# Performance work log

Hardware: AMD Instinct MI355X
Metric: run time of the kernel (lower is better)

Reference implementation:

```python
import jax, jax.numpy as jnp
import numpy as np

B, P, M = 16, 16384, 2048
D_Z, D_PHI, D_R = 512, 256, 64
H1, H2 = 96, 96
IN_DIM = D_Z + 3 * D_PHI + D_R  # 1344


def setup_inputs() -> dict:
    key = jax.random.key(0)
    ks = jax.random.split(key, 8)
    g_q = jax.random.normal(ks[0], (B, D_Z), dtype=jnp.float32)
    Phi = jax.random.normal(ks[1], (M, D_PHI), dtype=jnp.float32)
    # pair indices with i < j (sort each row)
    pi = jax.random.randint(ks[2], (P, 2), 0, M, dtype=jnp.int64)
    pair_index = jnp.sort(pi, axis=-1)
    relation_features = jax.random.normal(ks[3], (P, D_R), dtype=jnp.float32)
    # learned MLP params (Linear weights stored [in, out])
    W1 = jax.random.normal(ks[4], (IN_DIM, H1), dtype=jnp.float32) / np.sqrt(IN_DIM)
    b1 = jnp.zeros((H1,), dtype=jnp.float32)
    W2 = jax.random.normal(ks[5], (H1, H2), dtype=jnp.float32) / np.sqrt(H1)
    b2 = jnp.zeros((H2,), dtype=jnp.float32)
    W3 = jax.random.normal(ks[6], (H2, 1), dtype=jnp.float32) / np.sqrt(H2)
    b3 = jnp.zeros((1,), dtype=jnp.float32)
    return {"g_q": g_q, "Phi": Phi, "pair_index": pair_index,
            "relation_features": relation_features,
            "W1": W1, "b1": b1, "W2": W2, "b2": b2, "W3": W3, "b3": b3}


def reference(g_q, Phi, pair_index, relation_features, W1, b1, W2, b2, W3, b3):
    # gather pair embeddings: [P, d_phi]
    phi_i = Phi[pair_index[:, 0]]
    phi_j = Phi[pair_index[:, 1]]
    # symmetric combine -> [P, 3*d_phi + d_r]
    pair_feats = jnp.concatenate(
        [phi_i + phi_j, jnp.abs(phi_i - phi_j), phi_i * phi_j, relation_features],
        axis=-1)
    b, p = g_q.shape[0], pair_feats.shape[0]
    # broadcast-concat -> x: [B, P, in_dim]
    x = jnp.concatenate(
        [jnp.broadcast_to(g_q[:, None, :], (b, p, g_q.shape[-1])),
         jnp.broadcast_to(pair_feats[None, :, :], (b, p, pair_feats.shape[-1]))],
        axis=-1)
    # small MLP: Linear -> GELU (erf, dropout is identity at eval) x2, then Linear(->1)
    h = jax.nn.gelu(x @ W1 + b1, approximate=False)
    h = jax.nn.gelu(h @ W2 + b2, approximate=False)
    out = h @ W3 + b3  # [B, P, 1]
    return out[..., 0]  # [B, P]
```

## Files before the change

### kernel.cpp

```cpp
#include <hip/hip_runtime.h>
#include <hip/hip_bf16.h>
#include <stdint.h>

static constexpr int P_N   = 16384;
static constexpr int D_Z   = 512;
static constexpr int D_PHI = 256;
static constexpr int D_R   = 64;
static constexpr int H     = 96;
static constexpr int KP    = 832;

using f32x4 = __attribute__((ext_vector_type(4))) float;
using s16x8 = __attribute__((ext_vector_type(8))) short;

__device__ __forceinline__ unsigned short f2bf(float f) {
    union { float f; uint32_t u; } v; v.f = f;
    return (unsigned short)((v.u + 0x7FFFu + ((v.u >> 16) & 1u)) >> 16);
}

__device__ __forceinline__ uint32_t pkbf2(float lo, float hi) {
    union { __hip_bfloat162 h; uint32_t u; } c;
    c.h = __float22bfloat162_rn(make_float2(lo, hi));
    return c.u;
}

__device__ __forceinline__ float gelu_f(float x) {
    float x2 = x * x;
    float u  = __builtin_fmaf(-0.1029444f, x2, -2.3022126f);
    float e  = __builtin_amdgcn_exp2f(x * u);
    return x * __builtin_amdgcn_rcpf(1.0f + e);
}

__global__ __launch_bounds__(256) void prep_kernel(
    const float* __restrict__ g_q, const float* __restrict__ W1,
    const float* __restrict__ b1, const float* __restrict__ W2,
    float* __restrict__ gqfrag, unsigned short* __restrict__ W1frag,
    unsigned short* __restrict__ W2frag)
{
    __shared__ float gql[D_Z];
    __shared__ float red[192];
    const int blk = blockIdx.x;
    const int t = threadIdx.x;
    if (blk < 16) {
        const int b = blk;
        for (int i = t; i < D_Z; i += 256) gql[i] = g_q[b * D_Z + i];
        __syncthreads();
        float acc = 0.f;
        if (t < 192) {
            const int n = t % 96, s = t / 96;
            const int k0 = s * 256;
            #pragma unroll 8
            for (int k = 0; k < 256; ++k)
                acc += gql[k0 + k] * W1[(k0 + k) * H + n];
            red[t] = acc;
        }
        __syncthreads();
        if (t < 96) {
            const float v = red[t] + red[t + 96] + b1[t];
            const int dst = ((t >> 5) * 64 + ((t >> 3) & 3) * 16 + b) * 8 + (t & 7);
            gqfrag[dst] = v;
        }
    } else if (blk < 328) {
        const int e = (blk - 16) * 256 + t;
        const int n = e / KP, k = e % KP;
        const int nf = n >> 4, lr = n & 15;
        const int kc = k >> 5, l4 = (k >> 3) & 3, ke = k & 7;
        W1frag[((nf * 26 + kc) * 64 + l4 * 16 + lr) * 8 + ke] =
            f2bf(W1[(D_Z + k) * H + n]);
    } else {
        const int e = (blk - 328) * 256 + t;
        const int n = e / H, k = e % H;
        const int nf = n >> 4, lr = n & 15;
        const int ks = k >> 5, l4 = (k >> 3) & 3, ke = k & 7;
        W2frag[((nf * 3 + ks) * 64 + l4 * 16 + lr) * 8 + ke] =
            f2bf(W2[k * H + n]);
    }
}

__global__ __launch_bounds__(256, 4) void fused5_kernel(
    const float* __restrict__ Phi, const int* __restrict__ pidx,
    const float* __restrict__ rel, const unsigned short* __restrict__ W1frag,
    const float* __restrict__ gqfrag, const unsigned short* __restrict__ W2frag,
    const float* __restrict__ b2, const float* __restrict__ W3,
    const float* __restrict__ b3, float* __restrict__ out)
{
    constexpr int FS = 840;
    __shared__ __align__(16) unsigned short feats[8 * FS];
    __shared__ __align__(16) float y1part[2][8][96];
    const int t = threadIdx.x;
    const int p0 = blockIdx.x * 8;

    for (int task = t; task < 832; task += 256) {
        const int pair = task / 104;
        const int k = (task - pair * 104) * 8;
        float f[8];
        if (k < 768) {
            const int2 ij = *(const int2*)(pidx + 2 * (p0 + pair));
            const int kb = k & 255;
            const float* PI = Phi + ij.x * D_PHI + kb;
            const float* PJ = Phi + ij.y * D_PHI + kb;
            float4 a0 = *(const float4*)PI, a1 = *(const float4*)(PI + 4);
            float4 c0 = *(const float4*)PJ, c1 = *(const float4*)(PJ + 4);
            if (k < 256) {
                f[0]=a0.x+c0.x; f[1]=a0.y+c0.y; f[2]=a0.z+c0.z; f[3]=a0.w+c0.w;
                f[4]=a1.x+c1.x; f[5]=a1.y+c1.y; f[6]=a1.z+c1.z; f[7]=a1.w+c1.w;
            } else if (k < 512) {
                f[0]=fabsf(a0.x-c0.x); f[1]=fabsf(a0.y-c0.y); f[2]=fabsf(a0.z-c0.z); f[3]=fabsf(a0.w-c0.w);
                f[4]=fabsf(a1.x-c1.x); f[5]=fabsf(a1.y-c1.y); f[6]=fabsf(a1.z-c1.z); f[7]=fabsf(a1.w-c1.w);
            } else {
                f[0]=a0.x*c0.x; f[1]=a0.y*c0.y; f[2]=a0.z*c0.z; f[3]=a0.w*c0.w;
                f[4]=a1.x*c1.x; f[5]=a1.y*c1.y; f[6]=a1.z*c1.z; f[7]=a1.w*c1.w;
            }
        } else {
            const float* R = rel + (p0 + pair) * D_R + (k - 768);
            float4 a0 = *(const float4*)R, a1 = *(const float4*)(R + 4);
            f[0]=a0.x; f[1]=a0.y; f[2]=a0.z; f[3]=a0.w;
            f[4]=a1.x; f[5]=a1.y; f[6]=a1.z; f[7]=a1.w;
        }
        uint4 pk;
        pk.x = pkbf2(f[0], f[1]);
        pk.y = pkbf2(f[2], f[3]);
        pk.z = pkbf2(f[4], f[5]);
        pk.w = pkbf2(f[6], f[7]);
        *(uint4*)&feats[pair * FS + k] = pk;
    }
    __syncthreads();

    const int w  = t >> 6;
    const int l  = t & 63;
    const int lr = l & 15, l4 = l >> 4;

    {
        const int kh = w & 1, ng = w >> 1;
        f32x4 acc[3];
        acc[0] = (f32x4){0.f,0.f,0.f,0.f};
        acc[1] = (f32x4){0.f,0.f,0.f,0.f};
        acc[2] = (f32x4){0.f,0.f,0.f,0.f};
        const unsigned short* Arow = &feats[(lr & 7) * FS + l4 * 8];
        const int kc0 = kh * 13;
        for (int i = 0; i < 13; ++i) {
            const int kc = kc0 + i;
            const s16x8 a = *(const s16x8*)(Arow + kc * 32);
            #pragma unroll
            for (int j = 0; j < 3; ++j) {
                const s16x8 bb = *(const s16x8*)(W1frag +
                    (((ng * 3 + j) * 26 + kc) * 64 + l) * 8);
                acc[j] = __builtin_amdgcn_mfma_f32_16x16x32_bf16(a, bb, acc[j], 0, 0, 0);
            }
        }
        if (l4 < 2) {
            #pragma unroll
            for (int j = 0; j < 3; ++j)
                #pragma unroll
                for (int r = 0; r < 4; ++r)
                    y1part[kh][l4 * 4 + r][ng * 48 + j * 16 + lr] = acc[j][r];
        }
    }
    __syncthreads();

    s16x8 afr[2][3];
    #pragma unroll
    for (int ks = 0; ks < 3; ++ks) {
        const int c = ks * 32 + l4 * 8;
        const float* gp = gqfrag + (ks * 64 + l) * 8;
        float4 g0 = *(const float4*)gp, g1 = *(const float4*)(gp + 4);
        #pragma unroll
        for (int mf = 0; mf < 2; ++mf) {
            const int pl = 2 * w + mf;
            const float* ya = &y1part[0][pl][c];
            const float* yb = &y1part[1][pl][c];
            float4 u0 = *(const float4*)ya, u1 = *(const float4*)(ya + 4);
            float4 v0 = *(const float4*)yb, v1 = *(const float4*)(yb + 4);
            union { s16x8 v; uint32_t u[4]; } pk;
            pk.u[0] = pkbf2(gelu_f(g0.x + u0.x + v0.x), gelu_f(g0.y + u0.y + v0.y));
            pk.u[1] = pkbf2(gelu_f(g0.z + u0.z + v0.z), gelu_f(g0.w + u0.w + v0.w));
            pk.u[2] = pkbf2(gelu_f(g1.x + u1.x + v1.x), gelu_f(g1.y + u1.y + v1.y));
            pk.u[3] = pkbf2(gelu_f(g1.z + u1.z + v1.z), gelu_f(g1.w + u1.w + v1.w));
            afr[mf][ks] = pk.v;
        }
    }

    f32x4 acc2[2][6];
    #pragma unroll
    for (int nf = 0; nf < 6; ++nf) {
        const float bv = b2[nf * 16 + lr];
        acc2[0][nf] = (f32x4){bv, bv, bv, bv};
        acc2[1][nf] = (f32x4){bv, bv, bv, bv};
    }
    #pragma unroll
    for (int ks = 0; ks < 3; ++ks) {
        #pragma unroll
        for (int nf = 0; nf < 6; ++nf) {
            const s16x8 bb = *(const s16x8*)(W2frag + ((nf * 3 + ks) * 64 + l) * 8);
            acc2[0][nf] = __builtin_amdgcn_mfma_f32_16x16x32_bf16(afr[0][ks], bb, acc2[0][nf], 0, 0, 0);
            acc2[1][nf] = __builtin_amdgcn_mfma_f32_16x16x32_bf16(afr[1][ks], bb, acc2[1][nf], 0, 0, 0);
        }
    }

    float part[2][4] = {{0.f,0.f,0.f,0.f},{0.f,0.f,0.f,0.f}};
    #pragma unroll
    for (int nf = 0; nf < 6; ++nf) {
        const float wv = W3[nf * 16 + lr];
        #pragma unroll
        for (int mf = 0; mf < 2; ++mf)
            #pragma unroll
            for (int r4 = 0; r4 < 4; ++r4)
                part[mf][r4] = __builtin_fmaf(gelu_f(acc2[mf][nf][r4]), wv, part[mf][r4]);
    }
    #pragma unroll
    for (int mask = 1; mask <= 8; mask <<= 1)
        #pragma unroll
        for (int mf = 0; mf < 2; ++mf)
            #pragma unroll
            for (int r4 = 0; r4 < 4; ++r4)
                part[mf][r4] += __shfl_xor(part[mf][r4], mask, 64);
    if (lr == 0) {
        const float b3v = b3[0];
        #pragma unroll
        for (int mf = 0; mf < 2; ++mf)
            #pragma unroll
            for (int r4 = 0; r4 < 4; ++r4)
                out[(l4 * 4 + r4) * P_N + p0 + 2 * w + mf] = part[mf][r4] + b3v;
    }
}

extern "C" void kernel_launch(void* const* d_in, const int* in_sizes, int n_in,
                              void* d_out, int out_size, void* d_ws, size_t ws_size,
                              hipStream_t stream)
{
    const float* g_q  = (const float*)d_in[0];
    const float* Phi  = (const float*)d_in[1];
    const int*   pidx = (const int*)d_in[2];
    const float* rel  = (const float*)d_in[3];
    const float* W1   = (const float*)d_in[4];
    const float* b1   = (const float*)d_in[5];
    const float* W2   = (const float*)d_in[6];
    const float* b2   = (const float*)d_in[7];
    const float* W3   = (const float*)d_in[8];
    const float* b3   = (const float*)d_in[9];
    float* out = (float*)d_out;

    char* ws = (char*)d_ws;
    float*          gqfrag = (float*)(ws + 0);
    unsigned short* W1frag = (unsigned short*)(ws + 8192);
    unsigned short* W2frag = (unsigned short*)(ws + 167936);

    hipLaunchKernelGGL(prep_kernel, dim3(364), dim3(256), 0, stream,
                       g_q, W1, b1, W2, gqfrag, W1frag, W2frag);
    hipLaunchKernelGGL(fused5_kernel, dim3(P_N / 8), dim3(256), 0, stream,
                       Phi, pidx, rel, W1frag, gqfrag, W2frag, b2, W3, b3, out);
}
```

Before: 46.68 us.

## Split fused kernel into pair-side layer-1 GEMM and separate MLP kernel

Splits the fused kernel in two. The first kernel gathers features for 16 pairs per block, so all 16 rows of each MFMA tile are used (previously only 8). Each of its 6 waves owns one 16-column output fragment over the full K range, which removes the split-K partial sums and the shared-memory reduction. The pair-side layer-1 results go to a global workspace, and a second kernel reads them, adds the g_q term, and runs GELU, layer 2 and layer 3. In exchange it adds a kernel launch and a global round trip of the intermediate activations (P×96 floats).

```diff
diff --git a/kernel.cpp b/kernel.cpp
--- a/kernel.cpp
+++ b/kernel.cpp
@@ -76,20 +76,17 @@
     }
 }
 
-__global__ __launch_bounds__(256, 4) void fused5_kernel(
+__global__ __launch_bounds__(384, 4) void pair1_kernel(
     const float* __restrict__ Phi, const int* __restrict__ pidx,
     const float* __restrict__ rel, const unsigned short* __restrict__ W1frag,
-    const float* __restrict__ gqfrag, const unsigned short* __restrict__ W2frag,
-    const float* __restrict__ b2, const float* __restrict__ W3,
-    const float* __restrict__ b3, float* __restrict__ out)
+    float* __restrict__ y1p)
 {
     constexpr int FS = 840;
-    __shared__ __align__(16) unsigned short feats[8 * FS];
-    __shared__ __align__(16) float y1part[2][8][96];
+    __shared__ __align__(16) unsigned short feats[16 * FS];
     const int t = threadIdx.x;
-    const int p0 = blockIdx.x * 8;
-
-    for (int task = t; task < 832; task += 256) {
+    const int p0 = blockIdx.x * 16;
+
+    for (int task = t; task < 1664; task += 384) {
         const int pair = task / 104;
         const int k = (task - pair * 104) * 8;
         float f[8];
@@ -129,33 +126,30 @@
     const int l  = t & 63;
     const int lr = l & 15, l4 = l >> 4;
 
-    {
-        const int kh = w & 1, ng = w >> 1;
-        f32x4 acc[3];
-        acc[0] = (f32x4){0.f,0.f,0.f,0.f};
-        acc[1] = (f32x4){0.f,0.f,0.f,0.f};
-        acc[2] = (f32x4){0.f,0.f,0.f,0.f};
-        const unsigned short* Arow = &feats[(lr & 7) * FS + l4 * 8];
-        const int kc0 = kh * 13;
-        for (int i = 0; i < 13; ++i) {
-            const int kc = kc0 + i;
-            const s16x8 a = *(const s16x8*)(Arow + kc * 32);
-            #pragma unroll
-            for (int j = 0; j < 3; ++j) {
-                const s16x8 bb = *(const s16x8*)(W1frag +
-                    (((ng * 3 + j) * 26 + kc) * 64 + l) * 8);
-                acc[j] = __builtin_amdgcn_mfma_f32_16x16x32_bf16(a, bb, acc[j], 0, 0, 0);
-            }
-        }
-        if (l4 < 2) {
-            #pragma unroll
-            for (int j = 0; j < 3; ++j)
-                #pragma unroll
-                for (int r = 0; r < 4; ++r)
-                    y1part[kh][l4 * 4 + r][ng * 48 + j * 16 + lr] = acc[j][r];
-        }
-    }
-    __syncthreads();
+    f32x4 acc = (f32x4){0.f, 0.f, 0.f, 0.f};
+    const unsigned short* Arow = &feats[lr * FS + l4 * 8];
+    const unsigned short* Bb   = W1frag + (w * 26 * 64 + l) * 8;
+    #pragma unroll 2
+    for (int kc = 0; kc < 26; ++kc) {
+        const s16x8 a  = *(const s16x8*)(Arow + kc * 32);
+        const s16x8 bb = *(const s16x8*)(Bb + kc * 512);
+        acc = __builtin_amdgcn_mfma_f32_16x16x32_bf16(a, bb, acc, 0, 0, 0);
+    }
+    #pragma unroll
+    for (int r = 0; r < 4; ++r)
+        y1p[(p0 + l4 * 4 + r) * H + w * 16 + lr] = acc[r];
+}
+
+__global__ __launch_bounds__(256, 4) void mlp_kernel(
+    const float* __restrict__ gqfrag, const float* __restrict__ y1p,
+    const unsigned short* __restrict__ W2frag, const float* __restrict__ b2,
+    const float* __restrict__ W3, const float* __restrict__ b3,
+    float* __restrict__ out)
+{
+    const int t = threadIdx.x;
+    const int w = t >> 6, l = t & 63;
+    const int lr = l & 15, l4 = l >> 4;
+    const int p0 = blockIdx.x * 8;
 
     s16x8 afr[2][3];
     #pragma unroll
@@ -165,16 +159,13 @@
         float4 g0 = *(const float4*)gp, g1 = *(const float4*)(gp + 4);
         #pragma unroll
         for (int mf = 0; mf < 2; ++mf) {
-            const int pl = 2 * w + mf;
-            const float* ya = &y1part[0][pl][c];
-            const float* yb = &y1part[1][pl][c];
-            float4 u0 = *(const float4*)ya, u1 = *(const float4*)(ya + 4);
-            float4 v0 = *(const float4*)yb, v1 = *(const float4*)(yb + 4);
+            const float* yp = y1p + (p0 + 2 * w + mf) * H + c;
+            float4 u0 = *(const float4*)yp, u1 = *(const float4*)(yp + 4);
             union { s16x8 v; uint32_t u[4]; } pk;
-            pk.u[0] = pkbf2(gelu_f(g0.x + u0.x + v0.x), gelu_f(g0.y + u0.y + v0.y));
-            pk.u[1] = pkbf2(gelu_f(g0.z + u0.z + v0.z), gelu_f(g0.w + u0.w + v0.w));
-            pk.u[2] = pkbf2(gelu_f(g1.x + u1.x + v1.x), gelu_f(g1.y + u1.y + v1.y));
-            pk.u[3] = pkbf2(gelu_f(g1.z + u1.z + v1.z), gelu_f(g1.w + u1.w + v1.w));
+            pk.u[0] = pkbf2(gelu_f(g0.x + u0.x), gelu_f(g0.y + u0.y));
+            pk.u[1] = pkbf2(gelu_f(g0.z + u0.z), gelu_f(g0.w + u0.w));
+            pk.u[2] = pkbf2(gelu_f(g1.x + u1.x), gelu_f(g1.y + u1.y));
+            pk.u[3] = pkbf2(gelu_f(g1.z + u1.z), gelu_f(g1.w + u1.w));
             afr[mf][ks] = pk.v;
         }
     }
@@ -243,9 +234,12 @@
     float*          gqfrag = (float*)(ws + 0);
     unsigned short* W1frag = (unsigned short*)(ws + 8192);
     unsigned short* W2frag = (unsigned short*)(ws + 167936);
+    float*          y1p    = (float*)(ws + 196608);
 
     hipLaunchKernelGGL(prep_kernel, dim3(364), dim3(256), 0, stream,
                        g_q, W1, b1, W2, gqfrag, W1frag, W2frag);
-    hipLaunchKernelGGL(fused5_kernel, dim3(P_N / 8), dim3(256), 0, stream,
-                       Phi, pidx, rel, W1frag, gqfrag, W2frag, b2, W3, b3, out);
-}
+    hipLaunchKernelGGL(pair1_kernel, dim3(P_N / 16), dim3(384), 0, stream,
+                       Phi, pidx, rel, W1frag, y1p);
+    hipLaunchKernelGGL(mlp_kernel, dim3(P_N / 8), dim3(256), 0, stream,
+                       gqfrag, y1p, W2frag, b2, W3, b3, out);
+}
```

New measurement: 52.07 us. 1.12x slower.

## Process 16 pairs per 512-thread block to fill MFMA rows, split K four ways

Applied to the files above, without the earlier changes.

Each block now handles 16 pairs instead of 8, so the layer-1 MFMA A operand uses all 16 rows instead of duplicating 8. This halves W1 fragment traffic per pair. The K dimension is split across four waves (7/7/6/6 chunks), with the four partial sums reduced in shared memory. Layer 2 is restructured to loop over the pair fragments one at a time, which lowers live accumulator registers. The cost is more shared memory per block, fewer resident blocks, and extra partial-sum reads.

```diff
diff --git a/kernel.cpp b/kernel.cpp
--- a/kernel.cpp
+++ b/kernel.cpp
@@ -76,7 +76,7 @@
     }
 }
 
-__global__ __launch_bounds__(256, 4) void fused5_kernel(
+__global__ __launch_bounds__(512, 2) void fused9_kernel(
     const float* __restrict__ Phi, const int* __restrict__ pidx,
     const float* __restrict__ rel, const unsigned short* __restrict__ W1frag,
     const float* __restrict__ gqfrag, const unsigned short* __restrict__ W2frag,
@@ -84,20 +84,20 @@
     const float* __restrict__ b3, float* __restrict__ out)
 {
     constexpr int FS = 840;
-    __shared__ __align__(16) unsigned short feats[8 * FS];
-    __shared__ __align__(16) float y1part[2][8][96];
+    __shared__ __align__(16) unsigned short feats[16 * FS];
+    __shared__ __align__(16) float y1part[4][16][100];
     const int t = threadIdx.x;
-    const int p0 = blockIdx.x * 8;
-
-    for (int task = t; task < 832; task += 256) {
+    const int p0 = blockIdx.x * 16;
+
+    for (int task = t; task < 1664; task += 512) {
         const int pair = task / 104;
         const int k = (task - pair * 104) * 8;
         float f[8];
         if (k < 768) {
             const int2 ij = *(const int2*)(pidx + 2 * (p0 + pair));
             const int kb = k & 255;
-            const float* PI = Phi + ij.x * D_PHI + kb;
-            const float* PJ = Phi + ij.y * D_PHI + kb;
+            const float* PI = Phi + (long)ij.x * D_PHI + kb;
+            const float* PJ = Phi + (long)ij.y * D_PHI + kb;
             float4 a0 = *(const float4*)PI, a1 = *(const float4*)(PI + 4);
             float4 c0 = *(const float4*)PJ, c1 = *(const float4*)(PJ + 4);
             if (k < 256) {
@@ -111,7 +111,7 @@
                 f[4]=a1.x*c1.x; f[5]=a1.y*c1.y; f[6]=a1.z*c1.z; f[7]=a1.w*c1.w;
             }
         } else {
-            const float* R = rel + (p0 + pair) * D_R + (k - 768);
+            const float* R = rel + (long)(p0 + pair) * D_R + (k - 768);
             float4 a0 = *(const float4*)R, a1 = *(const float4*)(R + 4);
             f[0]=a0.x; f[1]=a0.y; f[2]=a0.z; f[3]=a0.w;
             f[4]=a1.x; f[5]=a1.y; f[6]=a1.z; f[7]=a1.w;
@@ -130,15 +130,15 @@
     const int lr = l & 15, l4 = l >> 4;
 
     {
-        const int kh = w & 1, ng = w >> 1;
+        const int kq = w & 3, ng = w >> 2;
+        const int kc_lo = (kq < 2) ? kq * 7 : 14 + (kq - 2) * 6;
+        const int kc_hi = (kq < 2) ? kc_lo + 7 : kc_lo + 6;
         f32x4 acc[3];
         acc[0] = (f32x4){0.f,0.f,0.f,0.f};
         acc[1] = (f32x4){0.f,0.f,0.f,0.f};
         acc[2] = (f32x4){0.f,0.f,0.f,0.f};
-        const unsigned short* Arow = &feats[(lr & 7) * FS + l4 * 8];
-        const int kc0 = kh * 13;
-        for (int i = 0; i < 13; ++i) {
-            const int kc = kc0 + i;
+        const unsigned short* Arow = &feats[lr * FS + l4 * 8];
+        for (int kc = kc_lo; kc < kc_hi; ++kc) {
             const s16x8 a = *(const s16x8*)(Arow + kc * 32);
             #pragma unroll
             for (int j = 0; j < 3; ++j) {
@@ -147,65 +147,67 @@
                 acc[j] = __builtin_amdgcn_mfma_f32_16x16x32_bf16(a, bb, acc[j], 0, 0, 0);
             }
         }
-        if (l4 < 2) {
-            #pragma unroll
-            for (int j = 0; j < 3; ++j)
-                #pragma unroll
-                for (int r = 0; r < 4; ++r)
-                    y1part[kh][l4 * 4 + r][ng * 48 + j * 16 + lr] = acc[j][r];
-        }
+        #pragma unroll
+        for (int j = 0; j < 3; ++j)
+            #pragma unroll
+            for (int r = 0; r < 4; ++r)
+                y1part[kq][l4 * 4 + r][ng * 48 + j * 16 + lr] = acc[j][r];
     }
     __syncthreads();
 
-    s16x8 afr[2][3];
+    float part[2][4];
     #pragma unroll
-    for (int ks = 0; ks < 3; ++ks) {
-        const int c = ks * 32 + l4 * 8;
-        const float* gp = gqfrag + (ks * 64 + l) * 8;
-        float4 g0 = *(const float4*)gp, g1 = *(const float4*)(gp + 4);
-        #pragma unroll
-        for (int mf = 0; mf < 2; ++mf) {
-            const int pl = 2 * w + mf;
-            const float* ya = &y1part[0][pl][c];
-            const float* yb = &y1part[1][pl][c];
-            float4 u0 = *(const float4*)ya, u1 = *(const float4*)(ya + 4);
-            float4 v0 = *(const float4*)yb, v1 = *(const float4*)(yb + 4);
+    for (int mf = 0; mf < 2; ++mf) {
+        const int pl = 2 * w + mf;
+
+        s16x8 afr[3];
+        #pragma unroll
+        for (int ks = 0; ks < 3; ++ks) {
+            const int c = ks * 32 + l4 * 8;
+            const float* gp = gqfrag + (ks * 64 + l) * 8;
+            float4 g0 = *(const float4*)gp, g1 = *(const float4*)(gp + 4);
+            float s0x=g0.x, s0y=g0.y, s0z=g0.z, s0w=g0.w;
+            float s1x=g1.x, s1y=g1.y, s1z=g1.z, s1w=g1.w;
+            #pragma unroll
+            for (int kq = 0; kq < 4; ++kq) {
+                const float* yp = &y1part[kq][pl][c];
+                float4 u0 = *(const float4*)yp, u1 = *(const float4*)(yp + 4);
+                s0x += u0.x; s0y += u0.y; s0z += u0.z; s0w += u0.w;
+                s1x += u1.x; s1y += u1.y; s1z += u1.z; s1w += u1.w;
+            }
             union { s16x8 v; uint32_t u[4]; } pk;
-            pk.u[0] = pkbf2(gelu_f(g0.x + u0.x + v0.x), gelu_f(g0.y + u0.y + v0.y));
-            pk.u[1] = pkbf2(gelu_f(g0.z + u0.z + v0.z), gelu_f(g0.w + u0.w + v0.w));
-            pk.u[2] = pkbf2(gelu_f(g1.x + u1.x + v1.x), gelu_f(g1.y + u1.y + v1.y));
-            pk.u[3] = pkbf2(gelu_f(g1.z + u1.z + v1.z), gelu_f(g1.w + u1.w + v1.w));
-            afr[mf][ks] = pk.v;
-        }
-    }
-
-    f32x4 acc2[2][6];
-    #pragma unroll
-    for (int nf = 0; nf < 6; ++nf) {
-        const float bv = b2[nf * 16 + lr];
-        acc2[0][nf] = (f32x4){bv, bv, bv, bv};
-        acc2[1][nf] = (f32x4){bv, bv, bv, bv};
-    }
-    #pragma unroll
-    for (int ks = 0; ks < 3; ++ks) {
+            pk.u[0] = pkbf2(gelu_f(s0x), gelu_f(s0y));
+            pk.u[1] = pkbf2(gelu_f(s0z), gelu_f(s0w));
+            pk.u[2] = pkbf2(gelu_f(s1x), gelu_f(s1y));
+            pk.u[3] = pkbf2(gelu_f(s1z), gelu_f(s1w));
+            afr[ks] = pk.v;
+        }
+
+        f32x4 acc2[6];
         #pragma unroll
         for (int nf = 0; nf < 6; ++nf) {
-            const s16x8 bb = *(const s16x8*)(W2frag + ((nf * 3 + ks) * 64 + l) * 8);
-            acc2[0][nf] = __builtin_amdgcn_mfma_f32_16x16x32_bf16(afr[0][ks], bb, acc2[0][nf], 0, 0, 0);
-            acc2[1][nf] = __builtin_amdgcn_mfma_f32_16x16x32_bf16(afr[1][ks], bb, acc2[1][nf], 0, 0, 0);
-        }
-    }
-
-    float part[2][4] = {{0.f,0.f,0.f,0.f},{0.f,0.f,0.f,0.f}};
-    #pragma unroll
-    for (int nf = 0; nf < 6; ++nf) {
-        const float wv = W3[nf * 16 + lr];
-        #pragma unroll
-        for (int mf = 0; mf < 2; ++mf)
+            const float bv = b2[nf * 16 + lr];
+            acc2[nf] = (f32x4){bv, bv, bv, bv};
+        }
+        #pragma unroll
+        for (int ks = 0; ks < 3; ++ks) {
+            #pragma unroll
+            for (int nf = 0; nf < 6; ++nf) {
+                const s16x8 bb = *(const s16x8*)(W2frag + ((nf * 3 + ks) * 64 + l) * 8);
+                acc2[nf] = __builtin_amdgcn_mfma_f32_16x16x32_bf16(afr[ks], bb, acc2[nf], 0, 0, 0);
+            }
+        }
+
+        part[mf][0] = part[mf][1] = part[mf][2] = part[mf][3] = 0.f;
+        #pragma unroll
+        for (int nf = 0; nf < 6; ++nf) {
+            const float wv = W3[nf * 16 + lr];
             #pragma unroll
             for (int r4 = 0; r4 < 4; ++r4)
-                part[mf][r4] = __builtin_fmaf(gelu_f(acc2[mf][nf][r4]), wv, part[mf][r4]);
-    }
+                part[mf][r4] = __builtin_fmaf(gelu_f(acc2[nf][r4]), wv, part[mf][r4]);
+        }
+    }
+
     #pragma unroll
     for (int mask = 1; mask <= 8; mask <<= 1)
         #pragma unroll
@@ -246,6 +248,6 @@
 
     hipLaunchKernelGGL(prep_kernel, dim3(364), dim3(256), 0, stream,
                        g_q, W1, b1, W2, gqfrag, W1frag, W2frag);
-    hipLaunchKernelGGL(fused5_kernel, dim3(P_N / 8), dim3(256), 0, stream,
+    hipLaunchKernelGGL(fused9_kernel, dim3(P_N / 16), dim3(512), 0, stream,
                        Phi, pidx, rel, W1frag, gqfrag, W2frag, b2, W3, b3, out);
 }
```

Result: faster. 44.06 us (-5.6%).
